# Kernel tuning notes

Measured on AMD Instinct MI355X. Metric: run time of the kernel, lower is better.

## Reference

```python
import jax, jax.numpy as jnp
import numpy as np

TEMPERATURE = 1.0

def _cauchy_kernel(x, y, temperature):
    # pairwise squared distances via Gram trick: ||x_i - y_j||^2
    sq_x = jnp.sum(x * x, axis=1)  # [n]
    sq_y = jnp.sum(y * y, axis=1)  # [m]
    d2 = sq_x[:, None] + sq_y[None, :] - 2.0 * (x @ y.T)
    d2 = jnp.maximum(d2, 0.0)
    return 1.0 / (1.0 + d2 / temperature)


def setup_inputs() -> dict:
    key = jax.random.key(0)
    k1, k2 = jax.random.split(key)
    features = jax.random.normal(k1, (8192, 128), dtype=jnp.float32)
    labels = jax.random.randint(k2, (8192,), 0, 1000, dtype=jnp.int64)
    return {"features": features, "labels": labels}


def reference(features, labels):
    b = features.shape[0] // 2
    z1 = features[:b]
    z2 = features[b:]
    z11 = _cauchy_kernel(z1, z1, TEMPERATURE)  # [b,b]
    z22 = _cauchy_kernel(z2, z2, TEMPERATURE)  # [b,b]
    z12 = _cauchy_kernel(z1, z2, TEMPERATURE)  # [b,b]

    eye = jnp.eye(b, dtype=z11.dtype)
    # positive term: mean log of matched-pair kernel (diagonal of z12)
    pos = jnp.sum(jnp.log(jnp.diagonal(z12))) / b
    # negative terms: row sums over [z11 - I | z12] and [z12^T | z22 - I]
    n1 = jnp.mean(jnp.log((z11 - eye).sum(axis=1) + z12.sum(axis=1)))
    n2 = jnp.mean(jnp.log(z12.sum(axis=0) + (z22 - eye).sum(axis=1)))
    neg = (n1 + n2) / 2.0
    return -(pos - neg)
```

## Files before the change

kernel.cpp:

```cpp
#include <hip/hip_runtime.h>
#include <math.h>

#define N_TOTAL 8192
#define BHALF   4096
#define KDIM    128

typedef __bf16 bf16x8 __attribute__((ext_vector_type(8)));
typedef __bf16 bf16x2 __attribute__((ext_vector_type(2)));
typedef float  f32x4  __attribute__((ext_vector_type(4)));

#define GLOAD_LDS16(GSRC, LDST)                                                \
    __builtin_amdgcn_global_load_lds(                                          \
        (const __attribute__((address_space(1))) void*)(GSRC),                 \
        (__attribute__((address_space(3))) void*)(LDST), 16, 0, 0)

__global__ __launch_bounds__(256) void k_prep_pos(const float* __restrict__ F,
                                                  __bf16* __restrict__ Fbf,
                                                  float* __restrict__ sq,
                                                  float* __restrict__ T,
                                                  float* __restrict__ out) {
    int t = threadIdx.x;
    int w = t >> 6, l = t & 63;
    int p = blockIdx.x * 4 + w;
    const float2* r1 = (const float2*)(F + (size_t)p * KDIM);
    const float2* r2 = (const float2*)(F + (size_t)(p + BHALF) * KDIM);
    float2 a = r1[l];
    float2 c = r2[l];

    float s1 = fmaf(a.x, a.x, a.y * a.y);
    float s2 = fmaf(c.x, c.x, c.y * c.y);
    float dp = fmaf(a.x, c.x, a.y * c.y);
#pragma unroll
    for (int off = 32; off > 0; off >>= 1) {
        s1 += __shfl_down(s1, off);
        s2 += __shfl_down(s2, off);
        dp += __shfl_down(dp, off);
    }

    bf16x2 pa, pc;
    pa[0] = (__bf16)a.x; pa[1] = (__bf16)a.y;
    pc[0] = (__bf16)c.x; pc[1] = (__bf16)c.y;
    ((bf16x2*)(Fbf + (size_t)p * KDIM))[l] = pa;
    ((bf16x2*)(Fbf + (size_t)(p + BHALF) * KDIM))[l] = pc;

    __shared__ float posRed[4];
    if (l == 0) {
        sq[p] = s1;
        sq[p + BHALF] = s2;
        T[p] = 0.0f;
        T[p + BHALF] = 0.0f;
        float d2 = fmaxf(s1 + s2 - 2.0f * dp, 0.0f);
        posRed[w] = logf(1.0f + d2);
    }
    __syncthreads();
    if (t == 0) {
        float s = posRed[0] + posRed[1] + posRed[2] + posRed[3];
        atomicAdd(out, s / (float)BHALF);
    }
}

__global__ __launch_bounds__(512, 4) void k_pairwise(
        const __bf16* __restrict__ Fbf,
        const float* __restrict__ sq,
        float* __restrict__ T) {
    int b = blockIdx.x;
    int ti = (int)floorf((129.0f - sqrtf(16641.0f - 8.0f * (float)b)) * 0.5f);
    while (ti * (129 - ti) / 2 > b) --ti;
    while ((ti + 1) * (128 - ti) / 2 <= b) ++ti;
    int tj = ti + (b - ti * (129 - ti) / 2);
    int I = ti * 128, J = tj * 128;
    bool diag = (ti == tj);

    __shared__ __align__(16) __bf16 As[128 * 128];
    __shared__ __align__(16) __bf16 Bs[128 * 128];
    __shared__ float rowAcc[128][2];
    __shared__ float colAcc[128][4];

    int t = threadIdx.x;
    int w = t >> 6;
    int l = t & 63;
    int wr = w >> 1, wc = w & 1;
    int low = l & 15, kb = l >> 4;

    const __bf16* FA = Fbf + (size_t)I * KDIM;
    const __bf16* FB = Fbf + (size_t)J * KDIM;
#pragma unroll
    for (int it = 0; it < 4; ++it) {
        int f = it * 512 + t;
        int row = f >> 4;
        int sg = f & 15;
        int g = sg ^ (row & 15);
        GLOAD_LDS16(FA + row * KDIM + g * 8, As + (size_t)f * 8);
        GLOAD_LDS16(FB + row * KDIM + g * 8, Bs + (size_t)f * 8);
    }
    __syncthreads();

    const bf16x8* Asg = (const bf16x8*)As;
    const bf16x8* Bsg = (const bf16x8*)Bs;
    f32x4 acc[2][4] = {};
#pragma unroll
    for (int s = 0; s < 4; ++s) {
        int g = s * 4 + kb;
        bf16x8 aF[2], bF[4];
#pragma unroll
        for (int fr = 0; fr < 2; ++fr) {
            int R = wr * 32 + fr * 16 + low;
            aF[fr] = Asg[R * 16 + (g ^ low)];
        }
#pragma unroll
        for (int fc = 0; fc < 4; ++fc) {
            int C = wc * 64 + fc * 16 + low;
            bF[fc] = Bsg[C * 16 + (g ^ low)];
        }
#pragma unroll
        for (int fr = 0; fr < 2; ++fr)
#pragma unroll
            for (int fc = 0; fc < 4; ++fc)
                acc[fr][fc] = __builtin_amdgcn_mfma_f32_16x16x32_bf16(
                    aF[fr], bF[fc], acc[fr][fc], 0, 0, 0);
    }

    float sqi[2][4], sqj[4];
#pragma unroll
    for (int fr = 0; fr < 2; ++fr)
#pragma unroll
        for (int r = 0; r < 4; ++r)
            sqi[fr][r] = sq[I + wr * 32 + fr * 16 + kb * 4 + r];
#pragma unroll
    for (int fc = 0; fc < 4; ++fc)
        sqj[fc] = sq[J + wc * 64 + fc * 16 + low];

    float rowPart[2][4] = {};
    float colPart[4] = {0.f, 0.f, 0.f, 0.f};
#pragma unroll
    for (int fr = 0; fr < 2; ++fr) {
#pragma unroll
        for (int fc = 0; fc < 4; ++fc) {
#pragma unroll
            for (int r = 0; r < 4; ++r) {
                float d2 = sqi[fr][r] + sqj[fc] - 2.0f * acc[fr][fc][r];
                d2 = fmaxf(d2, 0.0f);
                float v = __builtin_amdgcn_rcpf(1.0f + d2);
                rowPart[fr][r] += v;
                colPart[fc] += v;
            }
        }
    }

#pragma unroll
    for (int fr = 0; fr < 2; ++fr)
#pragma unroll
        for (int r = 0; r < 4; ++r) {
            float x = rowPart[fr][r];
            x += __shfl_xor(x, 1);
            x += __shfl_xor(x, 2);
            x += __shfl_xor(x, 4);
            x += __shfl_xor(x, 8);
            if (low == 0)
                rowAcc[wr * 32 + fr * 16 + kb * 4 + r][wc] = x;
        }

#pragma unroll
    for (int fc = 0; fc < 4; ++fc) {
        float x = colPart[fc];
        x += __shfl_xor(x, 16);
        x += __shfl_xor(x, 32);
        if (kb == 0)
            colAcc[wc * 64 + fc * 16 + low][wr] = x;
    }
    __syncthreads();

    if (t < 128) {
        atomicAdd(&T[I + t], rowAcc[t][0] + rowAcc[t][1]);
    } else if (t < 256 && !diag) {
        int c = t - 128;
        atomicAdd(&T[J + c],
                  colAcc[c][0] + colAcc[c][1] + colAcc[c][2] + colAcc[c][3]);
    }
}

__global__ __launch_bounds__(256) void k_final(const float* __restrict__ T,
                                               float* __restrict__ out) {
    int t = threadIdx.x;
    int i = blockIdx.x * 256 + t;
    float s = logf(T[i] - 1.0f);
#pragma unroll
    for (int off = 32; off > 0; off >>= 1) s += __shfl_down(s, off);
    __shared__ float red[4];
    int w = t >> 6, l = t & 63;
    if (l == 0) red[w] = s;
    __syncthreads();
    if (t == 0) {
        float S = red[0] + red[1] + red[2] + red[3];
        atomicAdd(out, S / (2.0f * (float)BHALF));
    }
}

extern "C" void kernel_launch(void* const* d_in, const int* in_sizes, int n_in,
                              void* d_out, int out_size, void* d_ws, size_t ws_size,
                              hipStream_t stream) {
    const float* F = (const float*)d_in[0];
    float* out = (float*)d_out;

    char* ws = (char*)d_ws;
    __bf16* Fbf = (__bf16*)ws;
    float*  sq  = (float*)(ws + (size_t)N_TOTAL * KDIM * 2);
    float*  T   = sq + N_TOTAL;

    hipMemsetAsync(out, 0, sizeof(float), stream);

    k_prep_pos<<<BHALF / 4, 256, 0, stream>>>(F, Fbf, sq, T, out);

    int nTiles = N_TOTAL / 128;
    int nBlocks = nTiles * (nTiles + 1) / 2;
    k_pairwise<<<nBlocks, 512, 0, stream>>>(Fbf, sq, T);

    k_final<<<N_TOTAL / 256, 256, 0, stream>>>(T, out);
}
```

Measured before the change: 98.13 us.

## Make pairwise kernel persistent over tile runs and replace atomics with partial buffers

Result: faster. 85.65 us (-12.7%).

```diff
diff --git a/kernel.cpp b/kernel.cpp
--- a/kernel.cpp
+++ b/kernel.cpp
@@ -4,6 +4,9 @@
 #define N_TOTAL 8192
 #define BHALF   4096
 #define KDIM    128
+#define NTILE   64
+#define NTRI    2080
+#define NBLK_PW 512
 
 typedef __bf16 bf16x8 __attribute__((ext_vector_type(8)));
 typedef __bf16 bf16x2 __attribute__((ext_vector_type(2)));
@@ -17,7 +20,7 @@
 __global__ __launch_bounds__(256) void k_prep_pos(const float* __restrict__ F,
                                                   __bf16* __restrict__ Fbf,
                                                   float* __restrict__ sq,
-                                                  float* __restrict__ T,
+                                                  float* __restrict__ posPart,
                                                   float* __restrict__ out) {
     int t = threadIdx.x;
     int w = t >> 6, l = t & 63;
@@ -47,30 +50,20 @@
     if (l == 0) {
         sq[p] = s1;
         sq[p + BHALF] = s2;
-        T[p] = 0.0f;
-        T[p + BHALF] = 0.0f;
         float d2 = fmaxf(s1 + s2 - 2.0f * dp, 0.0f);
         posRed[w] = logf(1.0f + d2);
     }
     __syncthreads();
     if (t == 0) {
-        float s = posRed[0] + posRed[1] + posRed[2] + posRed[3];
-        atomicAdd(out, s / (float)BHALF);
+        posPart[blockIdx.x] = posRed[0] + posRed[1] + posRed[2] + posRed[3];
+        if (blockIdx.x == 0) out[0] = 0.0f;
     }
 }
 
 __global__ __launch_bounds__(512, 4) void k_pairwise(
         const __bf16* __restrict__ Fbf,
         const float* __restrict__ sq,
-        float* __restrict__ T) {
-    int b = blockIdx.x;
-    int ti = (int)floorf((129.0f - sqrtf(16641.0f - 8.0f * (float)b)) * 0.5f);
-    while (ti * (129 - ti) / 2 > b) --ti;
-    while ((ti + 1) * (128 - ti) / 2 <= b) ++ti;
-    int tj = ti + (b - ti * (129 - ti) / 2);
-    int I = ti * 128, J = tj * 128;
-    bool diag = (ti == tj);
-
+        float* __restrict__ Tpart) {
     __shared__ __align__(16) __bf16 As[128 * 128];
     __shared__ __align__(16) __bf16 Bs[128 * 128];
     __shared__ float rowAcc[128][2];
@@ -82,117 +75,153 @@
     int wr = w >> 1, wc = w & 1;
     int low = l & 15, kb = l >> 4;
 
-    const __bf16* FA = Fbf + (size_t)I * KDIM;
-    const __bf16* FB = Fbf + (size_t)J * KDIM;
-#pragma unroll
-    for (int it = 0; it < 4; ++it) {
-        int f = it * 512 + t;
-        int row = f >> 4;
-        int sg = f & 15;
-        int g = sg ^ (row & 15);
-        GLOAD_LDS16(FA + row * KDIM + g * 8, As + (size_t)f * 8);
-        GLOAD_LDS16(FB + row * KDIM + g * 8, Bs + (size_t)f * 8);
-    }
-    __syncthreads();
-
-    const bf16x8* Asg = (const bf16x8*)As;
-    const bf16x8* Bsg = (const bf16x8*)Bs;
-    f32x4 acc[2][4] = {};
-#pragma unroll
-    for (int s = 0; s < 4; ++s) {
-        int g = s * 4 + kb;
-        bf16x8 aF[2], bF[4];
+    int bid = blockIdx.x;
+    int start = bid * 4 + (bid < 32 ? bid : 32);
+    int cnt = (bid < 32) ? 5 : 4;
+
+    int ti = (int)floorf((129.0f - sqrtf(16641.0f - 8.0f * (float)start)) * 0.5f);
+    while (ti * (129 - ti) / 2 > start) --ti;
+    while ((ti + 1) * (128 - ti) / 2 <= start) ++ti;
+    int tj = ti + (start - ti * (129 - ti) / 2);
+
+    int curTi = -1;
+#pragma unroll 1
+    for (int n = 0; n < cnt; ++n) {
+        int I = ti * 128, J = tj * 128;
+        bool diag = (ti == tj);
+
+        if (ti != curTi) {
+            const __bf16* FA = Fbf + (size_t)I * KDIM;
+#pragma unroll
+            for (int it = 0; it < 4; ++it) {
+                int f = it * 512 + t;
+                int row = f >> 4;
+                int sg = f & 15;
+                int g = sg ^ (row & 15);
+                GLOAD_LDS16(FA + row * KDIM + g * 8, As + (size_t)f * 8);
+            }
+            curTi = ti;
+        }
+        if (!diag) {
+            const __bf16* FB = Fbf + (size_t)J * KDIM;
+#pragma unroll
+            for (int it = 0; it < 4; ++it) {
+                int f = it * 512 + t;
+                int row = f >> 4;
+                int sg = f & 15;
+                int g = sg ^ (row & 15);
+                GLOAD_LDS16(FB + row * KDIM + g * 8, Bs + (size_t)f * 8);
+            }
+        }
+        __syncthreads();
+
+        const bf16x8* Asg = (const bf16x8*)As;
+        const bf16x8* Bsg = diag ? (const bf16x8*)As : (const bf16x8*)Bs;
+        f32x4 acc[2][4] = {};
+#pragma unroll
+        for (int s = 0; s < 4; ++s) {
+            int g = s * 4 + kb;
+            bf16x8 aF[2], bF[4];
+#pragma unroll
+            for (int fr = 0; fr < 2; ++fr) {
+                int R = wr * 32 + fr * 16 + low;
+                aF[fr] = Asg[R * 16 + (g ^ low)];
+            }
+#pragma unroll
+            for (int fc = 0; fc < 4; ++fc) {
+                int C = wc * 64 + fc * 16 + low;
+                bF[fc] = Bsg[C * 16 + (g ^ low)];
+            }
+#pragma unroll
+            for (int fr = 0; fr < 2; ++fr)
+#pragma unroll
+                for (int fc = 0; fc < 4; ++fc)
+                    acc[fr][fc] = __builtin_amdgcn_mfma_f32_16x16x32_bf16(
+                        aF[fr], bF[fc], acc[fr][fc], 0, 0, 0);
+        }
+
+        float sqi[2][4], sqj[4];
+#pragma unroll
+        for (int fr = 0; fr < 2; ++fr)
+#pragma unroll
+            for (int r = 0; r < 4; ++r)
+                sqi[fr][r] = sq[I + wr * 32 + fr * 16 + kb * 4 + r];
+#pragma unroll
+        for (int fc = 0; fc < 4; ++fc)
+            sqj[fc] = sq[J + wc * 64 + fc * 16 + low];
+
+        float rowPart[2][4] = {};
+        float colPart[4] = {0.f, 0.f, 0.f, 0.f};
 #pragma unroll
         for (int fr = 0; fr < 2; ++fr) {
-            int R = wr * 32 + fr * 16 + low;
-            aF[fr] = Asg[R * 16 + (g ^ low)];
-        }
+#pragma unroll
+            for (int fc = 0; fc < 4; ++fc) {
+#pragma unroll
+                for (int r = 0; r < 4; ++r) {
+                    float d2 = sqi[fr][r] + sqj[fc] - 2.0f * acc[fr][fc][r];
+                    d2 = fmaxf(d2, 0.0f);
+                    float v = __builtin_amdgcn_rcpf(1.0f + d2);
+                    rowPart[fr][r] += v;
+                    colPart[fc] += v;
+                }
+            }
+        }
+
+#pragma unroll
+        for (int fr = 0; fr < 2; ++fr)
+#pragma unroll
+            for (int r = 0; r < 4; ++r) {
+                float x = rowPart[fr][r];
+                x += __shfl_xor(x, 1);
+                x += __shfl_xor(x, 2);
+                x += __shfl_xor(x, 4);
+                x += __shfl_xor(x, 8);
+                if (low == 0)
+                    rowAcc[wr * 32 + fr * 16 + kb * 4 + r][wc] = x;
+            }
+
 #pragma unroll
         for (int fc = 0; fc < 4; ++fc) {
-            int C = wc * 64 + fc * 16 + low;
-            bF[fc] = Bsg[C * 16 + (g ^ low)];
-        }
-#pragma unroll
-        for (int fr = 0; fr < 2; ++fr)
-#pragma unroll
-            for (int fc = 0; fc < 4; ++fc)
-                acc[fr][fc] = __builtin_amdgcn_mfma_f32_16x16x32_bf16(
-                    aF[fr], bF[fc], acc[fr][fc], 0, 0, 0);
-    }
-
-    float sqi[2][4], sqj[4];
-#pragma unroll
-    for (int fr = 0; fr < 2; ++fr)
-#pragma unroll
-        for (int r = 0; r < 4; ++r)
-            sqi[fr][r] = sq[I + wr * 32 + fr * 16 + kb * 4 + r];
-#pragma unroll
-    for (int fc = 0; fc < 4; ++fc)
-        sqj[fc] = sq[J + wc * 64 + fc * 16 + low];
-
-    float rowPart[2][4] = {};
-    float colPart[4] = {0.f, 0.f, 0.f, 0.f};
-#pragma unroll
-    for (int fr = 0; fr < 2; ++fr) {
-#pragma unroll
-        for (int fc = 0; fc < 4; ++fc) {
-#pragma unroll
-            for (int r = 0; r < 4; ++r) {
-                float d2 = sqi[fr][r] + sqj[fc] - 2.0f * acc[fr][fc][r];
-                d2 = fmaxf(d2, 0.0f);
-                float v = __builtin_amdgcn_rcpf(1.0f + d2);
-                rowPart[fr][r] += v;
-                colPart[fc] += v;
-            }
-        }
-    }
-
-#pragma unroll
-    for (int fr = 0; fr < 2; ++fr)
-#pragma unroll
-        for (int r = 0; r < 4; ++r) {
-            float x = rowPart[fr][r];
-            x += __shfl_xor(x, 1);
-            x += __shfl_xor(x, 2);
-            x += __shfl_xor(x, 4);
-            x += __shfl_xor(x, 8);
-            if (low == 0)
-                rowAcc[wr * 32 + fr * 16 + kb * 4 + r][wc] = x;
-        }
-
-#pragma unroll
-    for (int fc = 0; fc < 4; ++fc) {
-        float x = colPart[fc];
-        x += __shfl_xor(x, 16);
-        x += __shfl_xor(x, 32);
-        if (kb == 0)
-            colAcc[wc * 64 + fc * 16 + low][wr] = x;
-    }
-    __syncthreads();
-
-    if (t < 128) {
-        atomicAdd(&T[I + t], rowAcc[t][0] + rowAcc[t][1]);
-    } else if (t < 256 && !diag) {
-        int c = t - 128;
-        atomicAdd(&T[J + c],
-                  colAcc[c][0] + colAcc[c][1] + colAcc[c][2] + colAcc[c][3]);
-    }
-}
-
-__global__ __launch_bounds__(256) void k_final(const float* __restrict__ T,
+            float x = colPart[fc];
+            x += __shfl_xor(x, 16);
+            x += __shfl_xor(x, 32);
+            if (kb == 0)
+                colAcc[wc * 64 + fc * 16 + low][wr] = x;
+        }
+        __syncthreads();
+
+        if (t < 128) {
+            Tpart[tj * N_TOTAL + I + t] = rowAcc[t][0] + rowAcc[t][1];
+        } else if (t < 256 && !diag) {
+            int c = t - 128;
+            Tpart[ti * N_TOTAL + J + c] =
+                colAcc[c][0] + colAcc[c][1] + colAcc[c][2] + colAcc[c][3];
+        }
+
+        ++tj;
+        if (tj == NTILE) { ++ti; tj = ti; }
+    }
+}
+
+__global__ __launch_bounds__(256) void k_final(const float* __restrict__ Tpart,
+                                               const float* __restrict__ posPart,
                                                float* __restrict__ out) {
     int t = threadIdx.x;
     int i = blockIdx.x * 256 + t;
-    float s = logf(T[i] - 1.0f);
-#pragma unroll
-    for (int off = 32; off > 0; off >>= 1) s += __shfl_down(s, off);
+    float s = 0.0f;
+#pragma unroll 8
+    for (int k = 0; k < NTILE; ++k) s += Tpart[k * N_TOTAL + i];
+    float v = logf(s - 1.0f);
+    if (t < 32) v += 2.0f * posPart[blockIdx.x * 32 + t];
+#pragma unroll
+    for (int off = 32; off > 0; off >>= 1) v += __shfl_down(v, off);
     __shared__ float red[4];
     int w = t >> 6, l = t & 63;
-    if (l == 0) red[w] = s;
+    if (l == 0) red[w] = v;
     __syncthreads();
     if (t == 0) {
         float S = red[0] + red[1] + red[2] + red[3];
-        atomicAdd(out, S / (2.0f * (float)BHALF));
+        atomicAdd(out, S * (1.0f / (2.0f * (float)BHALF)));
     }
 }
 
@@ -203,17 +232,12 @@
     float* out = (float*)d_out;
 
     char* ws = (char*)d_ws;
-    __bf16* Fbf = (__bf16*)ws;
-    float*  sq  = (float*)(ws + (size_t)N_TOTAL * KDIM * 2);
-    float*  T   = sq + N_TOTAL;
-
-    hipMemsetAsync(out, 0, sizeof(float), stream);
-
-    k_prep_pos<<<BHALF / 4, 256, 0, stream>>>(F, Fbf, sq, T, out);
-
-    int nTiles = N_TOTAL / 128;
-    int nBlocks = nTiles * (nTiles + 1) / 2;
-    k_pairwise<<<nBlocks, 512, 0, stream>>>(Fbf, sq, T);
-
-    k_final<<<N_TOTAL / 256, 256, 0, stream>>>(T, out);
-}
+    __bf16* Fbf    = (__bf16*)ws;
+    float*  sq     = (float*)(ws + (size_t)N_TOTAL * KDIM * 2);
+    float*  posPart = sq + N_TOTAL;
+    float*  Tpart  = posPart + 1024;
+
+    k_prep_pos<<<BHALF / 4, 256, 0, stream>>>(F, Fbf, sq, posPart, out);
+    k_pairwise<<<NBLK_PW, 512, 0, stream>>>(Fbf, sq, Tpart);
+    k_final<<<N_TOTAL / 256, 256, 0, stream>>>(Tpart, posPart, out);
+}
```
